# Kernel optimization log

Measured on AMD Instinct MI355X. Metric: run time of the kernel, lower is better.

Reference implementation:

```python
import jax, jax.numpy as jnp
import numpy as np

RADIUS = 1.3
RES = 128
SH_DEG = 2
N_SH = (SH_DEG + 1) ** 2          # 9 SH basis functions
DATA_DIM = N_SH * 3 + 1           # 28: 27 SH rgb coeffs + 1 sigma
STEP = (2.0 * RADIUS / RES) / 2.0 # half a voxel, as in calc_step_size
N_INTRS = int(np.ceil(np.sqrt(3.0) * 2.0 * RES))  # torch.arange(float) length
N_RAYS = 4096


def sh_basis(d):
    # Real spherical harmonics up to degree 2, svox2/plenoxels convention. d: [B,3]
    x, y, z = d[:, 0], d[:, 1], d[:, 2]
    return jnp.stack([
        0.28209479177387814 * jnp.ones_like(x),
        -0.4886025119029199 * y,
        0.4886025119029199 * z,
        -0.4886025119029199 * x,
        1.0925484305920792 * x * y,
        -1.0925484305920792 * y * z,
        0.31539156525252005 * (2.0 * z * z - x * x - y * y),
        -1.0925484305920792 * x * z,
        0.5462742152960396 * (x * x - y * y),
    ], axis=-1)  # [B, 9]


def trilerp(grid, pts):
    # grid: [C, R, R, R] laid out (D,H,W); pts: [N,3] as (x,y,z) in [-1,1],
    # x indexes W, y indexes H, z indexes D (torch grid_sample convention),
    # align_corners=True, padding_mode='border'. Returns [C, N].
    R = grid.shape[-1]
    c = jnp.clip((pts + 1.0) * 0.5 * (R - 1), 0.0, R - 1)  # border padding
    c0 = jnp.floor(c)
    f = c - c0
    i0 = c0.astype(jnp.int32)
    i1 = jnp.minimum(i0 + 1, R - 1)
    x0, y0, z0 = i0[:, 0], i0[:, 1], i0[:, 2]
    x1, y1, z1 = i1[:, 0], i1[:, 1], i1[:, 2]
    fx, fy, fz = f[:, 0], f[:, 1], f[:, 2]
    g = lambda zi, yi, xi: grid[:, zi, yi, xi]  # [C, N]
    out = (g(z0, y0, x0) * ((1 - fz) * (1 - fy) * (1 - fx)) +
           g(z0, y0, x1) * ((1 - fz) * (1 - fy) * fx) +
           g(z0, y1, x0) * ((1 - fz) * fy * (1 - fx)) +
           g(z0, y1, x1) * ((1 - fz) * fy * fx) +
           g(z1, y0, x0) * (fz * (1 - fy) * (1 - fx)) +
           g(z1, y0, x1) * (fz * (1 - fy) * fx) +
           g(z1, y1, x0) * (fz * fy * (1 - fx)) +
           g(z1, y1, x1) * (fz * fy * fx))
    return out


def setup_inputs() -> dict:
    key = jax.random.key(0)
    k1, k2, k3 = jax.random.split(key, 3)
    rays_o = jax.random.normal(k1, (N_RAYS, 3), jnp.float32) * 0.3  # inside cube
    rd = jax.random.normal(k2, (N_RAYS, 3), jnp.float32)
    rays_d = rd / jnp.linalg.norm(rd, axis=-1, keepdims=True)
    # grid parameter: SH coeffs init 0.1, sigma init 0.01 (as in module) + noise
    base = jnp.concatenate([
        jnp.full((1, DATA_DIM - 1, RES, RES, RES), 0.1, jnp.float32),
        jnp.full((1, 1, RES, RES, RES), 0.01, jnp.float32)], axis=1)
    data = base + 0.01 * jax.random.normal(k3, (1, DATA_DIM, RES, RES, RES), jnp.float32)
    return {"rays_o": rays_o, "rays_d": rays_d, "data": data}


def reference(rays_o, rays_d, data):
    # --- ray/box intersection sampling (no grad in original) ---
    ro = jax.lax.stop_gradient(rays_o)
    rd = jax.lax.stop_gradient(rays_d)
    off_pos = (RADIUS - ro) / rd
    off_neg = (-RADIUS - ro) / rd
    start = jnp.max(jnp.minimum(off_pos, off_neg), axis=-1, keepdims=True)  # [B,1]
    steps = jnp.arange(N_INTRS, dtype=ro.dtype)[None, :]
    intersections = start + steps * STEP          # [B, N_INTRS]
    t = intersections[:, :-1]                     # [B, NI]
    pts = ro[:, None, :] + t[..., None] * rd[:, None, :]  # [B, NI, 3]
    mask = jnp.all((pts > -RADIUS) & (pts < RADIUS), axis=-1)  # [B, NI]
    ptsn = pts / RADIUS
    B, NI = t.shape

    # --- trilinear interpolation of grid at all sample points ---
    interp = trilerp(data[0], ptsn.reshape(-1, 3)).T  # [B*NI, 28]
    sigma = jax.nn.relu(interp[:, -1].reshape(B, NI))
    sigma = jnp.where(mask, sigma, 0.0)  # masked_scatter into zeros

    # --- sigma2alpha: standard volumetric compositing weights ---
    dists = (intersections[:, 1:] - intersections[:, :-1]) \
            * jnp.linalg.norm(rays_d, axis=-1, keepdims=True)  # [B, NI]
    alpha = 1.0 - jnp.exp(-sigma * dists)
    trans = jnp.cumprod(jnp.concatenate(
        [jnp.ones((B, 1), alpha.dtype), 1.0 - alpha + 1e-10], axis=1), axis=1)[:, :-1]
    abs_light = alpha * trans  # [B, NI]

    # --- SH -> rgb per sample ---
    sh_mult = sh_basis(rays_d)  # [B, 9]
    sh = interp[:, :-1].reshape(B, NI, 3, N_SH)
    rgb_pts = jnp.einsum('bk,bnck->bnc', sh_mult, sh)  # [B, NI, 3]
    rgb_pts = jnp.where(mask[..., None], rgb_pts, 0.0)  # masked_scatter

    # --- shrgb2rgb: sigmoid, composite, white background ---
    rgb = jnp.sum(abs_light[..., None] * jax.nn.sigmoid(rgb_pts), axis=1)  # [B,3]
    rgb = rgb + (1.0 - jnp.sum(abs_light, axis=1))[..., None]  # white bkgd
    return rgb
```

## Files before the change

kernel.cpp:

```cpp
#include <hip/hip_runtime.h>
#include <math.h>


typedef float f2v __attribute__((ext_vector_type(2)));

namespace {
constexpr float kRadius   = 1.3f;
constexpr int   kRes      = 128;
constexpr float kStep     = 2.0f * 1.3f / 128.0f / 2.0f;
constexpr int   kNI       = 443;
constexpr int   kNRays    = 4096;
constexpr int   kChStride = kRes * kRes * kRes;
constexpr int   kCh       = 28;
constexpr int   kRecBytes = 32;
constexpr size_t kVoxBytes = (size_t)kChStride * kRecBytes;
constexpr int   kChunks   = 2;
constexpr int   kChunks7  = 7;
}

__device__ __forceinline__ unsigned part1by2(unsigned v)
{
    v &= 0x7Fu;
    v = (v | (v << 16)) & 0x030000FFu;
    v = (v | (v <<  8)) & 0x0300F00Fu;
    v = (v | (v <<  4)) & 0x030C30C3u;
    v = (v | (v <<  2)) & 0x09249249u;
    return v;
}

__global__ __launch_bounds__(256)
void convert_grid(const float* __restrict__ grid, unsigned char* __restrict__ vox)
{
    const unsigned lin = blockIdx.x * 256 + threadIdx.x;
    const unsigned x = lin & 127u;
    const unsigned y = (lin >> 7) & 127u;
    const unsigned z = lin >> 14;
    const unsigned m = part1by2(x) | (part1by2(y) << 1) | (part1by2(z) << 2);

    float c[kCh];
    #pragma unroll
    for (int ch = 0; ch < kCh; ++ch)
        c[ch] = __builtin_nontemporal_load(grid + (size_t)ch * kChStride + lin);

    unsigned w[8];
    #pragma unroll
    for (int i = 0; i < 6; ++i) {
        int lo = __builtin_amdgcn_cvt_pk_fp8_f32(c[4*i],   c[4*i+1], 0,  false);
        w[i]   = (unsigned)__builtin_amdgcn_cvt_pk_fp8_f32(c[4*i+2], c[4*i+3], lo, true);
    }
    {
        int lo = __builtin_amdgcn_cvt_pk_fp8_f32(c[24], c[25], 0,  false);
        w[6]   = (unsigned)__builtin_amdgcn_cvt_pk_fp8_f32(c[26], 0.0f, lo, true);
    }
    {
        union { unsigned short u; _Float16 h; } cv;
        cv.h = (_Float16)c[27];
        w[7] = (unsigned)cv.u;
    }

    uint4* dst = (uint4*)(vox + (size_t)m * kRecBytes);
    dst[0] = make_uint4(w[0], w[1], w[2], w[3]);
    dst[1] = make_uint4(w[4], w[5], w[6], w[7]);
}

struct SampleC { float a, cR, cG, cB; };

__device__ __forceinline__ SampleC eval_sample(
    int k, float start, float ox, float oy, float oz,
    float dx, float dy, float dz, float dist,
    const float* __restrict__ shm, const unsigned char* __restrict__ vox)
{
    SampleC s;
    s.a = 1.f; s.cR = s.cG = s.cB = 0.f;
    if (k >= kNI) return s;

    const float t  = start + (float)k * kStep;
    const float px = ox + t*dx;
    const float py = oy + t*dy;
    const float pz = oz + t*dz;
    const bool inb = (px > -kRadius) && (px < kRadius) &&
                     (py > -kRadius) && (py < kRadius) &&
                     (pz > -kRadius) && (pz < kRadius);

    float alpha = 0.0f;
    if (inb) {
        const float cx = fminf(fmaxf((px*(1.0f/kRadius) + 1.0f)*0.5f*127.0f, 0.0f), 127.0f);
        const float cy = fminf(fmaxf((py*(1.0f/kRadius) + 1.0f)*0.5f*127.0f, 0.0f), 127.0f);
        const float cz = fminf(fmaxf((pz*(1.0f/kRadius) + 1.0f)*0.5f*127.0f, 0.0f), 127.0f);
        const float fx0 = floorf(cx), fy0 = floorf(cy), fz0 = floorf(cz);
        const float fx = cx - fx0, fy = cy - fy0, fz = cz - fz0;
        const int ix0 = (int)fx0, iy0 = (int)fy0, iz0 = (int)fz0;
        const int ix1 = min(ix0 + 1, 127);
        const int iy1 = min(iy0 + 1, 127);
        const int iz1 = min(iz0 + 1, 127);

        const float gx0 = 1.0f - fx, gy0 = 1.0f - fy, gz0 = 1.0f - fz;

        const unsigned X0 = part1by2((unsigned)ix0);
        const unsigned X1 = part1by2((unsigned)ix1);
        const unsigned Y0 = part1by2((unsigned)iy0) << 1;
        const unsigned Y1 = part1by2((unsigned)iy1) << 1;
        const unsigned Z0 = part1by2((unsigned)iz0) << 2;
        const unsigned Z1 = part1by2((unsigned)iz1) << 2;

        const unsigned offs[8] = {
            Z0 | Y0 | X0,  Z0 | Y0 | X1,  Z0 | Y1 | X0,  Z0 | Y1 | X1,
            Z1 | Y0 | X0,  Z1 | Y0 | X1,  Z1 | Y1 | X0,  Z1 | Y1 | X1 };
        const float cw[8] = {
            gz0*gy0*gx0, gz0*gy0*fx, gz0*fy*gx0, gz0*fy*fx,
            fz *gy0*gx0, fz *gy0*fx, fz *fy*gx0, fz *fy*fx };

        float rp0 = 0.f, rp1 = 0.f, rp2 = 0.f, sig = 0.f;
        #pragma unroll
        for (int cn = 0; cn < 8; ++cn) {
            const uint4* vp = (const uint4*)(vox + (size_t)offs[cn] * kRecBytes);
            const uint4 u0 = vp[0], u1 = vp[1];

            float f[28];
            const unsigned wd[7] = { u0.x, u0.y, u0.z, u0.w, u1.x, u1.y, u1.z };
            #pragma unroll
            for (int i = 0; i < 7; ++i) {
                const f2v lo = __builtin_amdgcn_cvt_pk_f32_fp8((int)wd[i], false);
                const f2v hi = __builtin_amdgcn_cvt_pk_f32_fp8((int)wd[i], true);
                f[4*i+0] = lo.x; f[4*i+1] = lo.y; f[4*i+2] = hi.x; f[4*i+3] = hi.y;
            }
            union { unsigned short u; _Float16 h; } cv;
            cv.u = (unsigned short)(u1.w & 0xffffu);
            const float sv = (float)cv.h;

            float r = 0.f, g = 0.f, b = 0.f;
            #pragma unroll
            for (int j = 0; j < 9; ++j) {
                r = fmaf(shm[j], f[j],      r);
                g = fmaf(shm[j], f[9 + j],  g);
                b = fmaf(shm[j], f[18 + j], b);
            }
            const float wc = cw[cn];
            rp0 = fmaf(wc, r, rp0);
            rp1 = fmaf(wc, g, rp1);
            rp2 = fmaf(wc, b, rp2);
            sig = fmaf(wc, sv, sig);
        }
        sig = fmaxf(sig, 0.0f);
        alpha = 1.0f - expf(-sig * dist);
        s.cR = alpha * (1.0f / (1.0f + expf(-rp0)));
        s.cG = alpha * (1.0f / (1.0f + expf(-rp1)));
        s.cB = alpha * (1.0f / (1.0f + expf(-rp2)));
    }
    s.a = 1.0f - alpha + 1e-10f;
    return s;
}

__device__ __forceinline__ float wave_scan_prod(float a, int lane, float& total)
{
    float prod = a;
    #pragma unroll
    for (int off = 1; off < 64; off <<= 1) {
        const float y = __shfl_up(prod, off, 64);
        if (lane >= off) prod *= y;
    }
    float excl = __shfl_up(prod, 1, 64);
    if (lane == 0) excl = 1.0f;
    total = __shfl(prod, 63, 64);
    return excl;
}

__global__ __launch_bounds__(256, 3)
void render_chunks(const float* __restrict__ rays_o,
                   const float* __restrict__ rays_d,
                   const unsigned char* __restrict__ vox,
                   float* __restrict__ partials)
{
    const int lane  = threadIdx.x & 63;
    const int W     = blockIdx.x * 4 + (threadIdx.x >> 6);
    const int ray   = W >> 1;
    const int chunk = W & 1;

    const float ox = rays_o[3*ray+0], oy = rays_o[3*ray+1], oz = rays_o[3*ray+2];
    const float dx = rays_d[3*ray+0], dy = rays_d[3*ray+1], dz = rays_d[3*ray+2];

    const float ppx = ( kRadius - ox)/dx, pnx = (-kRadius - ox)/dx;
    const float ppy = ( kRadius - oy)/dy, pny = (-kRadius - oy)/dy;
    const float ppz = ( kRadius - oz)/dz, pnz = (-kRadius - oz)/dz;
    const float start  = fmaxf(fminf(ppx, pnx), fmaxf(fminf(ppy, pny), fminf(ppz, pnz)));
    const float t_exit = fminf(fmaxf(ppx, pnx), fminf(fmaxf(ppy, pny), fmaxf(ppz, pnz)));

    const int base = chunk * 256;

    if (start + (float)base * kStep > t_exit + kStep) {
        if (lane == 0) {
            float* p = partials + (size_t)(ray * kChunks + chunk) * 5;
            p[0] = 0.f; p[1] = 0.f; p[2] = 0.f; p[3] = 0.f; p[4] = 1.f;
        }
        return;
    }

    const float dnorm = sqrtf(dx*dx + dy*dy + dz*dz);
    const float dist  = kStep * dnorm;

    float shm[9];
    shm[0] =  0.28209479177387814f;
    shm[1] = -0.4886025119029199f * dy;
    shm[2] =  0.4886025119029199f * dz;
    shm[3] = -0.4886025119029199f * dx;
    shm[4] =  1.0925484305920792f * dx * dy;
    shm[5] = -1.0925484305920792f * dy * dz;
    shm[6] =  0.31539156525252005f * (2.0f*dz*dz - dx*dx - dy*dy);
    shm[7] = -1.0925484305920792f * dx * dz;
    shm[8] =  0.5462742152960396f * (dx*dx - dy*dy);

    const SampleC A = eval_sample(base       + lane, start, ox, oy, oz, dx, dy, dz, dist, shm, vox);
    const SampleC B = eval_sample(base +  64 + lane, start, ox, oy, oz, dx, dy, dz, dist, shm, vox);
    const SampleC C = eval_sample(base + 128 + lane, start, ox, oy, oz, dx, dy, dz, dist, shm, vox);
    const SampleC D = eval_sample(base + 192 + lane, start, ox, oy, oz, dx, dy, dz, dist, shm, vox);

    float P0, P1, P2, P3;
    const float eA = wave_scan_prod(A.a, lane, P0);
    const float eB = wave_scan_prod(B.a, lane, P1);
    const float eC = wave_scan_prod(C.a, lane, P2);
    const float eD = wave_scan_prod(D.a, lane, P3);

    const float pA = eA;
    const float pB = P0 * eB;
    const float pC = P0 * P1 * eC;
    const float pD = P0 * P1 * P2 * eD;

    const float one = 1.0f + 1e-10f;
    float rL = pA * (one - A.a) + pB * (one - B.a)
             + pC * (one - C.a) + pD * (one - D.a);

    float rR = pA * A.cR;  rR = fmaf(pB, B.cR, rR);
    rR = fmaf(pC, C.cR, rR);  rR = fmaf(pD, D.cR, rR);
    float rG = pA * A.cG;  rG = fmaf(pB, B.cG, rG);
    rG = fmaf(pC, C.cG, rG);  rG = fmaf(pD, D.cG, rG);
    float rB = pA * A.cB;  rB = fmaf(pB, B.cB, rB);
    rB = fmaf(pC, C.cB, rB);  rB = fmaf(pD, D.cB, rB);

    const float P = P0 * P1 * P2 * P3;

    #pragma unroll
    for (int off = 32; off > 0; off >>= 1) {
        rR += __shfl_down(rR, off, 64);
        rG += __shfl_down(rG, off, 64);
        rB += __shfl_down(rB, off, 64);
        rL += __shfl_down(rL, off, 64);
    }

    if (lane == 0) {
        float* p = partials + (size_t)(ray * kChunks + chunk) * 5;
        p[0] = rR; p[1] = rG; p[2] = rB; p[3] = rL; p[4] = P;
    }
}

__global__ __launch_bounds__(256)
void combine_chunks(const float* __restrict__ partials, float* __restrict__ out)
{
    const int r = blockIdx.x * 256 + threadIdx.x;
    const float* p = partials + (size_t)r * (kChunks * 5);

    float carry = 1.0f, aR = 0.f, aG = 0.f, aB = 0.f, aL = 0.f;
    #pragma unroll
    for (int c = 0; c < kChunks; ++c) {
        aR = fmaf(carry, p[c*5 + 0], aR);
        aG = fmaf(carry, p[c*5 + 1], aG);
        aB = fmaf(carry, p[c*5 + 2], aB);
        aL = fmaf(carry, p[c*5 + 3], aL);
        carry *= p[c*5 + 4];
    }
    const float bg = 1.0f - aL;
    out[3*r + 0] = aR + bg;
    out[3*r + 1] = aG + bg;
    out[3*r + 2] = aB + bg;
}

#define TRI8(p) (w000*(p)[o000] + w001*(p)[o001] + w010*(p)[o010] + w011*(p)[o011] \
               + w100*(p)[o100] + w101*(p)[o101] + w110*(p)[o110] + w111*(p)[o111])

__global__ __launch_bounds__(256)
void plenoxel_render_direct(const float* __restrict__ rays_o,
                            const float* __restrict__ rays_d,
                            const float* __restrict__ grid,
                            float* __restrict__ out)
{
    const int lane = threadIdx.x & 63;
    const int ray  = blockIdx.x * 4 + (threadIdx.x >> 6);

    const float ox = rays_o[3*ray+0], oy = rays_o[3*ray+1], oz = rays_o[3*ray+2];
    const float dx = rays_d[3*ray+0], dy = rays_d[3*ray+1], dz = rays_d[3*ray+2];

    const float sx = fminf(( kRadius - ox)/dx, (-kRadius - ox)/dx);
    const float sy = fminf(( kRadius - oy)/dy, (-kRadius - oy)/dy);
    const float sz = fminf(( kRadius - oz)/dz, (-kRadius - oz)/dz);
    const float start = fmaxf(sx, fmaxf(sy, sz));
    const float dnorm = sqrtf(dx*dx + dy*dy + dz*dz);

    float shm[9];
    shm[0] =  0.28209479177387814f;
    shm[1] = -0.4886025119029199f * dy;
    shm[2] =  0.4886025119029199f * dz;
    shm[3] = -0.4886025119029199f * dx;
    shm[4] =  1.0925484305920792f * dx * dy;
    shm[5] = -1.0925484305920792f * dy * dz;
    shm[6] =  0.31539156525252005f * (2.0f*dz*dz - dx*dx - dy*dy);
    shm[7] = -1.0925484305920792f * dx * dz;
    shm[8] =  0.5462742152960396f * (dx*dx - dy*dy);

    float carry = 1.0f;
    float accR = 0.f, accG = 0.f, accB = 0.f, accL = 0.f;

    for (int chunk = 0; chunk < kChunks7; ++chunk) {
        const int k = chunk * 64 + lane;
        float alpha = 0.0f, a = 1.0f;
        float rp0 = 0.f, rp1 = 0.f, rp2 = 0.f;
        bool inb = false;

        if (k < kNI) {
            const float t = start + (float)k * kStep;
            const float dist = kStep * dnorm;
            const float px = ox + t*dx, py = oy + t*dy, pz = oz + t*dz;
            inb = (px > -kRadius) && (px < kRadius) &&
                  (py > -kRadius) && (py < kRadius) &&
                  (pz > -kRadius) && (pz < kRadius);
            float sigma = 0.0f;
            if (inb) {
                const float cx = fminf(fmaxf((px*(1.0f/kRadius) + 1.0f)*0.5f*127.0f, 0.0f), 127.0f);
                const float cy = fminf(fmaxf((py*(1.0f/kRadius) + 1.0f)*0.5f*127.0f, 0.0f), 127.0f);
                const float cz = fminf(fmaxf((pz*(1.0f/kRadius) + 1.0f)*0.5f*127.0f, 0.0f), 127.0f);
                const float fx0 = floorf(cx), fy0 = floorf(cy), fz0 = floorf(cz);
                const float fx = cx - fx0, fy = cy - fy0, fz = cz - fz0;
                const int ix0 = (int)fx0, iy0 = (int)fy0, iz0 = (int)fz0;
                const int ix1 = min(ix0 + 1, 127);
                const int iy1 = min(iy0 + 1, 127);
                const int iz1 = min(iz0 + 1, 127);
                const float gx0 = 1.0f - fx, gy0 = 1.0f - fy, gz0 = 1.0f - fz;
                const float w000 = gz0*gy0*gx0, w001 = gz0*gy0*fx;
                const float w010 = gz0*fy *gx0, w011 = gz0*fy *fx;
                const float w100 = fz *gy0*gx0, w101 = fz *gy0*fx;
                const float w110 = fz *fy *gx0, w111 = fz *fy *fx;
                const int o000 = iz0*(kRes*kRes) + iy0*kRes + ix0;
                const int o001 = iz0*(kRes*kRes) + iy0*kRes + ix1;
                const int o010 = iz0*(kRes*kRes) + iy1*kRes + ix0;
                const int o011 = iz0*(kRes*kRes) + iy1*kRes + ix1;
                const int o100 = iz1*(kRes*kRes) + iy0*kRes + ix0;
                const int o101 = iz1*(kRes*kRes) + iy0*kRes + ix1;
                const int o110 = iz1*(kRes*kRes) + iy1*kRes + ix0;
                const int o111 = iz1*(kRes*kRes) + iy1*kRes + ix1;
                #pragma unroll
                for (int kk = 0; kk < 9; ++kk) {
                    rp0 = fmaf(shm[kk], TRI8(grid + (kk     ) * kChStride), rp0);
                    rp1 = fmaf(shm[kk], TRI8(grid + (kk +  9) * kChStride), rp1);
                    rp2 = fmaf(shm[kk], TRI8(grid + (kk + 18) * kChStride), rp2);
                }
                sigma = fmaxf(TRI8(grid + 27 * kChStride), 0.0f);
            }
            alpha = 1.0f - expf(-sigma * dist);
            a     = 1.0f - alpha + 1e-10f;
        }

        float prod = a;
        #pragma unroll
        for (int off = 1; off < 64; off <<= 1) {
            const float y = __shfl_up(prod, off, 64);
            if (lane >= off) prod *= y;
        }
        float excl = __shfl_up(prod, 1, 64);
        if (lane == 0) excl = 1.0f;
        const float trans = carry * excl;
        const float w = alpha * trans;
        if (inb) {
            accR = fmaf(w, 1.0f / (1.0f + expf(-rp0)), accR);
            accG = fmaf(w, 1.0f / (1.0f + expf(-rp1)), accG);
            accB = fmaf(w, 1.0f / (1.0f + expf(-rp2)), accB);
        }
        accL += w;
        carry *= __shfl(prod, 63, 64);
    }

    #pragma unroll
    for (int off = 32; off > 0; off >>= 1) {
        accR += __shfl_down(accR, off, 64);
        accG += __shfl_down(accG, off, 64);
        accB += __shfl_down(accB, off, 64);
        accL += __shfl_down(accL, off, 64);
    }

    if (lane == 0) {
        const float bg = 1.0f - accL;
        out[3*ray + 0] = accR + bg;
        out[3*ray + 1] = accG + bg;
        out[3*ray + 2] = accB + bg;
    }
}

extern "C" void kernel_launch(void* const* d_in, const int* in_sizes, int n_in,
                              void* d_out, int out_size, void* d_ws, size_t ws_size,
                              hipStream_t stream) {
    const float* rays_o = (const float*)d_in[0];
    const float* rays_d = (const float*)d_in[1];
    const float* data   = (const float*)d_in[2];
    float* out = (float*)d_out;

    const size_t partBytes = (size_t)kNRays * kChunks * 5 * sizeof(float);
    const size_t need = kVoxBytes + partBytes;

    if (ws_size >= need) {
        unsigned char* vox = (unsigned char*)d_ws;
        float* partials = (float*)((char*)d_ws + kVoxBytes);

        hipLaunchKernelGGL(convert_grid,
                           dim3(kChStride / 256), dim3(256), 0, stream,
                           data, vox);
        hipLaunchKernelGGL(render_chunks,
                           dim3(kNRays * kChunks / 4), dim3(256), 0, stream,
                           rays_o, rays_d, vox, partials);
        hipLaunchKernelGGL(combine_chunks,
                           dim3(kNRays / 256), dim3(256), 0, stream,
                           partials, out);
    } else {
        hipLaunchKernelGGL(plenoxel_render_direct,
                           dim3(kNRays / 4), dim3(256), 0, stream,
                           rays_o, rays_d, data, out);
    }
}
```

Measured before the change: 361.0 us.

## Accumulate trilinear-weighted coefficients before SH dot, use packed FMAs and Morton LUT

The SH dot product moves out of the per-corner loop: the 28 decoded coefficients are first accumulated with trilinear weights into packed float2 accumulators, and the SH basis is applied once per sample. This cuts the per-corner FMA count and uses packed FMA instructions. Morton bit-interleaving now comes from a 128-entry shared-memory lookup table instead of per-sample bit twiddling, which adds a block barrier. The exponential and reciprocal switch to fast intrinsics, trading a little precision and raising register pressure from the 14 float2 accumulators.

Result: no change. 363.8 us (+0.8%).

```diff
diff --git a/kernel.cpp b/kernel.cpp
--- a/kernel.cpp
+++ b/kernel.cpp
@@ -65,10 +65,17 @@
 
 struct SampleC { float a, cR, cG, cB; };
 
+struct ShPack {
+    f2v p0, p1, p2, p3;
+    f2v g0, g1, g2, g3;
+    float s0, s8;
+};
+
 __device__ __forceinline__ SampleC eval_sample(
     int k, float start, float ox, float oy, float oz,
     float dx, float dy, float dz, float dist,
-    const float* __restrict__ shm, const unsigned char* __restrict__ vox)
+    const ShPack& sh, const unsigned char* __restrict__ vox,
+    const unsigned* __restrict__ mlut)
 {
     SampleC s;
     s.a = 1.f; s.cR = s.cG = s.cB = 0.f;
@@ -96,12 +103,12 @@
 
         const float gx0 = 1.0f - fx, gy0 = 1.0f - fy, gz0 = 1.0f - fz;
 
-        const unsigned X0 = part1by2((unsigned)ix0);
-        const unsigned X1 = part1by2((unsigned)ix1);
-        const unsigned Y0 = part1by2((unsigned)iy0) << 1;
-        const unsigned Y1 = part1by2((unsigned)iy1) << 1;
-        const unsigned Z0 = part1by2((unsigned)iz0) << 2;
-        const unsigned Z1 = part1by2((unsigned)iz1) << 2;
+        const unsigned X0 = mlut[ix0];
+        const unsigned X1 = mlut[ix1];
+        const unsigned Y0 = mlut[iy0] << 1;
+        const unsigned Y1 = mlut[iy1] << 1;
+        const unsigned Z0 = mlut[iz0] << 2;
+        const unsigned Z1 = mlut[iz1] << 2;
 
         const unsigned offs[8] = {
             Z0 | Y0 | X0,  Z0 | Y0 | X1,  Z0 | Y1 | X0,  Z0 | Y1 | X1,
@@ -110,42 +117,52 @@
             gz0*gy0*gx0, gz0*gy0*fx, gz0*fy*gx0, gz0*fy*fx,
             fz *gy0*gx0, fz *gy0*fx, fz *fy*gx0, fz *fy*fx };
 
-        float rp0 = 0.f, rp1 = 0.f, rp2 = 0.f, sig = 0.f;
+        f2v acc[14];
+        #pragma unroll
+        for (int i = 0; i < 14; ++i) acc[i] = (f2v){0.f, 0.f};
+        float sig = 0.f;
+
         #pragma unroll
         for (int cn = 0; cn < 8; ++cn) {
             const uint4* vp = (const uint4*)(vox + (size_t)offs[cn] * kRecBytes);
             const uint4 u0 = vp[0], u1 = vp[1];
 
-            float f[28];
+            const float wc = cw[cn];
+            const f2v wc2 = {wc, wc};
             const unsigned wd[7] = { u0.x, u0.y, u0.z, u0.w, u1.x, u1.y, u1.z };
             #pragma unroll
             for (int i = 0; i < 7; ++i) {
                 const f2v lo = __builtin_amdgcn_cvt_pk_f32_fp8((int)wd[i], false);
                 const f2v hi = __builtin_amdgcn_cvt_pk_f32_fp8((int)wd[i], true);
-                f[4*i+0] = lo.x; f[4*i+1] = lo.y; f[4*i+2] = hi.x; f[4*i+3] = hi.y;
+                acc[2*i]   = __builtin_elementwise_fma(wc2, lo, acc[2*i]);
+                acc[2*i+1] = __builtin_elementwise_fma(wc2, hi, acc[2*i+1]);
             }
             union { unsigned short u; _Float16 h; } cv;
             cv.u = (unsigned short)(u1.w & 0xffffu);
-            const float sv = (float)cv.h;
-
-            float r = 0.f, g = 0.f, b = 0.f;
-            #pragma unroll
-            for (int j = 0; j < 9; ++j) {
-                r = fmaf(shm[j], f[j],      r);
-                g = fmaf(shm[j], f[9 + j],  g);
-                b = fmaf(shm[j], f[18 + j], b);
-            }
-            const float wc = cw[cn];
-            rp0 = fmaf(wc, r, rp0);
-            rp1 = fmaf(wc, g, rp1);
-            rp2 = fmaf(wc, b, rp2);
-            sig = fmaf(wc, sv, sig);
+            sig = fmaf(wc, (float)cv.h, sig);
         }
-        sig = fmaxf(sig, 0.0f);
-        alpha = 1.0f - expf(-sig * dist);
-        s.cR = alpha * (1.0f / (1.0f + expf(-rp0)));
-        s.cG = alpha * (1.0f / (1.0f + expf(-rp1)));
-        s.cB = alpha * (1.0f / (1.0f + expf(-rp2)));
+
+        f2v rv = acc[0] * sh.p0;
+        rv = __builtin_elementwise_fma(acc[1], sh.p1, rv);
+        rv = __builtin_elementwise_fma(acc[2], sh.p2, rv);
+        rv = __builtin_elementwise_fma(acc[3], sh.p3, rv);
+        const float rp0 = rv.x + rv.y + sh.s8 * acc[4].x;
+        f2v gv = acc[5] * sh.g0;
+        gv = __builtin_elementwise_fma(acc[6], sh.g1, gv);
+        gv = __builtin_elementwise_fma(acc[7], sh.g2, gv);
+        gv = __builtin_elementwise_fma(acc[8], sh.g3, gv);
+        const float rp1 = gv.x + gv.y + sh.s0 * acc[4].y;
+        f2v bv = acc[9] * sh.p0;
+        bv = __builtin_elementwise_fma(acc[10], sh.p1, bv);
+        bv = __builtin_elementwise_fma(acc[11], sh.p2, bv);
+        bv = __builtin_elementwise_fma(acc[12], sh.p3, bv);
+        const float rp2 = bv.x + bv.y + sh.s8 * acc[13].x;
+
+        const float sgc = fmaxf(sig, 0.0f);
+        alpha = 1.0f - __expf(-sgc * dist);
+        s.cR = alpha * __builtin_amdgcn_rcpf(1.0f + __expf(-rp0));
+        s.cG = alpha * __builtin_amdgcn_rcpf(1.0f + __expf(-rp1));
+        s.cB = alpha * __builtin_amdgcn_rcpf(1.0f + __expf(-rp2));
     }
     s.a = 1.0f - alpha + 1e-10f;
     return s;
@@ -171,6 +188,10 @@
                    const unsigned char* __restrict__ vox,
                    float* __restrict__ partials)
 {
+    __shared__ unsigned mlut[128];
+    if (threadIdx.x < 128) mlut[threadIdx.x] = part1by2(threadIdx.x);
+    __syncthreads();
+
     const int lane  = threadIdx.x & 63;
     const int W     = blockIdx.x * 4 + (threadIdx.x >> 6);
     const int ray   = W >> 1;
@@ -198,21 +219,27 @@
     const float dnorm = sqrtf(dx*dx + dy*dy + dz*dz);
     const float dist  = kStep * dnorm;
 
-    float shm[9];
-    shm[0] =  0.28209479177387814f;
-    shm[1] = -0.4886025119029199f * dy;
-    shm[2] =  0.4886025119029199f * dz;
-    shm[3] = -0.4886025119029199f * dx;
-    shm[4] =  1.0925484305920792f * dx * dy;
-    shm[5] = -1.0925484305920792f * dy * dz;
-    shm[6] =  0.31539156525252005f * (2.0f*dz*dz - dx*dx - dy*dy);
-    shm[7] = -1.0925484305920792f * dx * dz;
-    shm[8] =  0.5462742152960396f * (dx*dx - dy*dy);
-
-    const SampleC A = eval_sample(base       + lane, start, ox, oy, oz, dx, dy, dz, dist, shm, vox);
-    const SampleC B = eval_sample(base +  64 + lane, start, ox, oy, oz, dx, dy, dz, dist, shm, vox);
-    const SampleC C = eval_sample(base + 128 + lane, start, ox, oy, oz, dx, dy, dz, dist, shm, vox);
-    const SampleC D = eval_sample(base + 192 + lane, start, ox, oy, oz, dx, dy, dz, dist, shm, vox);
+    const float m0 =  0.28209479177387814f;
+    const float m1 = -0.4886025119029199f * dy;
+    const float m2 =  0.4886025119029199f * dz;
+    const float m3 = -0.4886025119029199f * dx;
+    const float m4 =  1.0925484305920792f * dx * dy;
+    const float m5 = -1.0925484305920792f * dy * dz;
+    const float m6 =  0.31539156525252005f * (2.0f*dz*dz - dx*dx - dy*dy);
+    const float m7 = -1.0925484305920792f * dx * dz;
+    const float m8 =  0.5462742152960396f * (dx*dx - dy*dy);
+
+    ShPack sh;
+    sh.p0 = (f2v){m0, m1};  sh.p1 = (f2v){m2, m3};
+    sh.p2 = (f2v){m4, m5};  sh.p3 = (f2v){m6, m7};
+    sh.g0 = (f2v){m1, m2};  sh.g1 = (f2v){m3, m4};
+    sh.g2 = (f2v){m5, m6};  sh.g3 = (f2v){m7, m8};
+    sh.s0 = m0;  sh.s8 = m8;
+
+    const SampleC A = eval_sample(base       + lane, start, ox, oy, oz, dx, dy, dz, dist, sh, vox, mlut);
+    const SampleC B = eval_sample(base +  64 + lane, start, ox, oy, oz, dx, dy, dz, dist, sh, vox, mlut);
+    const SampleC C = eval_sample(base + 128 + lane, start, ox, oy, oz, dx, dy, dz, dist, sh, vox, mlut);
+    const SampleC D = eval_sample(base + 192 + lane, start, ox, oy, oz, dx, dy, dz, dist, sh, vox, mlut);
 
     float P0, P1, P2, P3;
     const float eA = wave_scan_prod(A.a, lane, P0);
```
